# Kernel tuning notes

Hardware: AMD Instinct MI355X
Metric: run time of the kernel (lower is better)

The kernel has to match this reference:

```python
import jax, jax.numpy as jnp
import numpy as np

S, B, H, E, V, T = 160, 64, 1024, 512, 64, 16


def setup_inputs() -> dict:
    key = jax.random.key(0)
    ks = jax.random.split(key, 13)
    g = lambda k, shape, scale: jax.random.normal(k, shape, jnp.float32) * scale
    return dict(
        encoder_h0=g(ks[0], (1, B, H), 1.0),
        encoder_c0=g(ks[1], (1, B, H), 1.0),
        encoder_outputs=g(ks[2], (S, B, H), 1.0),
        encoder_lens=jax.random.randint(ks[3], (B,), 1, S + 1),
        tok_embed=g(ks[4], (1, E), 0.02),
        embed=g(ks[5], (V, E), 0.02),
        W_ih=g(ks[6], (4 * H, E), 1.0 / np.sqrt(E)),
        W_hh=g(ks[7], (4 * H, H), 1.0 / np.sqrt(H)),
        b_ih=jnp.zeros((4 * H,), jnp.float32),
        b_hh=jnp.zeros((4 * H,), jnp.float32),
        out_W=g(ks[8], (V, 2 * H), 1.0 / np.sqrt(2 * H)),
        out_b=jnp.zeros((V,), jnp.float32),
        enc_W=g(ks[9], (H, H), 1.0 / np.sqrt(H)),
        enc_b=jnp.zeros((H,), jnp.float32),
        dec_W=g(ks[10], (H, H), 1.0 / np.sqrt(H)),
        dec_b=jnp.zeros((H,), jnp.float32),
        attn_W=g(ks[11], (1, H), 1.0 / np.sqrt(H)),
        attn_b=jnp.zeros((1,), jnp.float32),
    )


def reference(encoder_h0, encoder_c0, encoder_outputs, encoder_lens,
              tok_embed, embed, W_ih, W_hh, b_ih, b_hh,
              out_W, out_b, enc_W, enc_b, dec_W, dec_b, attn_W, attn_b):
    S_, B_, H_ = encoder_outputs.shape
    h0, c0 = encoder_h0[0], encoder_c0[0]          # [B,H]; source re-feeds encoder_hidden each step
    invalid = jnp.arange(S_)[None, :] >= encoder_lens[:, None]   # [B,S] True where masked
    NEG = jnp.float32(-1e9)

    def step(embed_tok, _):
        # LSTM cell, torch gate order (i, f, g, o)
        gates = embed_tok @ W_ih.T + b_ih + h0 @ W_hh.T + b_hh   # [B,4H]
        i, f, g, o = jnp.split(gates, 4, axis=-1)
        c = jax.nn.sigmoid(f) * c0 + jax.nn.sigmoid(i) * jnp.tanh(g)
        out = jax.nn.sigmoid(o) * jnp.tanh(c)                    # [B,H]
        # additive (Bahdanau) attention scores
        enc_t = jnp.einsum('sbh,kh->sbk', encoder_outputs, enc_W) + enc_b   # [S,B,H]
        dec_t = out @ dec_W.T + dec_b                                       # [B,H]
        scores = (jnp.tanh(enc_t + dec_t[None]) @ attn_W[0] + attn_b[0]).T # [B,S]
        attn = jax.nn.softmax(jnp.where(invalid, NEG, scores), axis=-1)    # [B,S]
        context = jnp.einsum('bs,sbh->bh', attn, encoder_outputs)          # [B,H]
        combined = jnp.concatenate([context, out], axis=-1)                # [B,2H]
        probs = jax.nn.softmax(combined @ out_W.T + out_b, axis=-1)
        probs = probs / jnp.sum(probs, axis=-1, keepdims=True)             # source renormalizes
        tok = jnp.argmax(probs, axis=-1)                                   # greedy decode
        onehot = jax.nn.one_hot(tok, probs.shape[-1], dtype=probs.dtype)
        neg_ent = jnp.sum(jax.lax.stop_gradient(probs) * jnp.log(probs + 1e-6), axis=-1)
        logp = jnp.log(jnp.sum(probs * onehot, axis=-1) + 1e-6)
        return embed[tok], (tok, attn, neg_ent, logp)

    start = jnp.broadcast_to(tok_embed[0], (B_, tok_embed.shape[1]))  # <SOS> embedding
    _, (toks, attns, negents, logps) = jax.lax.scan(step, start, None, length=T)
    predicted_tokens = toks                            # [T,B]
    context_total = jnp.transpose(attns, (1, 0, 2))    # [B,T,S] (attention maps, as in source)
    return predicted_tokens, context_total, jnp.sum(negents, axis=0), jnp.sum(logps, axis=0)
```

## Files before the change

kernel.cpp:

```cpp
#include <hip/hip_runtime.h>

#define S_ 160
#define B_ 64
#define H_ 1024
#define E_ 512
#define V_ 64
#define T_ 16
#define H4_ 4096

__device__ __forceinline__ float sigm(float x) { return 1.f / (1.f + expf(-x)); }

__global__ __launch_bounds__(512) void gemm_bt_128(
    const float* __restrict__ A, const float* __restrict__ Bm,
    const float* __restrict__ bias, float* __restrict__ Cd,
    int M, int N, int K)
{
    __shared__ float As[16][132];
    __shared__ float Bs[16][132];
    const int bn = blockIdx.x, bm = blockIdx.y;
    const int tid = threadIdx.x;
    const int lr = tid >> 2, lk = (tid & 3) * 4;
    const int cx4 = (tid & 15) * 4, ry4 = (tid >> 4) * 4;
    const float* Ap = A + (size_t)(bm * 128 + lr) * K + lk;
    const float* Bp = Bm + (size_t)(bn * 128 + lr) * K + lk;
    float acc[4][8] = {};
    for (int k0 = 0; k0 < K; k0 += 16) {
        float4 av = *(const float4*)(Ap + k0);
        float4 bv = *(const float4*)(Bp + k0);
        __syncthreads();
        As[lk + 0][lr] = av.x; As[lk + 1][lr] = av.y;
        As[lk + 2][lr] = av.z; As[lk + 3][lr] = av.w;
        Bs[lk + 0][lr] = bv.x; Bs[lk + 1][lr] = bv.y;
        Bs[lk + 2][lr] = bv.z; Bs[lk + 3][lr] = bv.w;
        __syncthreads();
#pragma unroll
        for (int kk = 0; kk < 16; ++kk) {
            float a[4], b[8];
            *(float4*)(a)     = *(const float4*)&As[kk][ry4];
            *(float4*)(b)     = *(const float4*)&Bs[kk][cx4];
            *(float4*)(b + 4) = *(const float4*)&Bs[kk][64 + cx4];
#pragma unroll
            for (int i = 0; i < 4; ++i)
#pragma unroll
                for (int j = 0; j < 8; ++j) acc[i][j] = fmaf(a[i], b[j], acc[i][j]);
        }
    }
#pragma unroll
    for (int i = 0; i < 4; ++i) {
        int row = bm * 128 + ry4 + i;
#pragma unroll
        for (int j = 0; j < 8; ++j) {
            int col = bn * 128 + ((j < 4) ? (cx4 + j) : (64 + cx4 + j - 4));
            Cd[(size_t)row * N + col] = acc[i][j] + bias[col];
        }
    }
}

__device__ __forceinline__ void tile64(const float* __restrict__ Arow,
                                       const float* __restrict__ Brow,
                                       int K, float acc[4][4],
                                       float* __restrict__ As,
                                       float* __restrict__ Bs)
{
    const int tid = threadIdx.x;
    const int lr = tid >> 2, lc = (tid & 3) << 2;
    const int tx = tid & 15, ty = tid >> 4;
    for (int k0 = 0; k0 < K; k0 += 16) {
        float4 av = *(const float4*)(Arow + k0);
        float4 bv = *(const float4*)(Brow + k0);
        __syncthreads();
        As[lr * 17 + lc + 0] = av.x; As[lr * 17 + lc + 1] = av.y;
        As[lr * 17 + lc + 2] = av.z; As[lr * 17 + lc + 3] = av.w;
        Bs[lr * 17 + lc + 0] = bv.x; Bs[lr * 17 + lc + 1] = bv.y;
        Bs[lr * 17 + lc + 2] = bv.z; Bs[lr * 17 + lc + 3] = bv.w;
        __syncthreads();
#pragma unroll
        for (int kk = 0; kk < 16; ++kk) {
            float a[4], b[4];
#pragma unroll
            for (int i = 0; i < 4; ++i) a[i] = As[(ty * 4 + i) * 17 + kk];
#pragma unroll
            for (int j = 0; j < 4; ++j) b[j] = Bs[(tx * 4 + j) * 17 + kk];
#pragma unroll
            for (int i = 0; i < 4; ++i)
#pragma unroll
                for (int j = 0; j < 4; ++j) acc[i][j] = fmaf(a[i], b[j], acc[i][j]);
        }
    }
    __syncthreads();
}

__global__ __launch_bounds__(256) void gemm_part(
    const float* __restrict__ A, const float* __restrict__ Bm,
    float* __restrict__ Cpart, int M, int N, int K)
{
    __shared__ float smem[2176];
    const int bn = blockIdx.x, bm = blockIdx.y, kz = blockIdx.z, KS = gridDim.z;
    const int tid = threadIdx.x;
    const int lr = tid >> 2, lc = (tid & 3) << 2;
    const int tx = tid & 15, ty = tid >> 4;
    const int kLen = K / KS, k0base = kz * kLen;
    float acc[4][4] = {};
    tile64(A + (size_t)(bm * 64 + lr) * K + k0base + lc,
           Bm + (size_t)(bn * 64 + lr) * K + k0base + lc,
           kLen, acc, smem, smem + 1088);
    float* Cp = Cpart + (size_t)kz * M * N;
#pragma unroll
    for (int i = 0; i < 4; ++i) {
        int row = bm * 64 + ty * 4 + i;
#pragma unroll
        for (int j = 0; j < 4; ++j)
            Cp[(size_t)row * N + bn * 64 + tx * 4 + j] = acc[i][j];
    }
}

__global__ void reduce_partials(const float* __restrict__ Cpart, int KS,
                                const float* __restrict__ bias,
                                const float* __restrict__ bias2,
                                float* __restrict__ C, int MN, int N)
{
    int idx = blockIdx.x * 256 + threadIdx.x;
    if (idx >= MN) return;
    float v = 0.f;
    for (int z = 0; z < KS; ++z) v += Cpart[(size_t)z * MN + idx];
    int col = idx % N;
    if (bias)  v += bias[col];
    if (bias2) v += bias2[col];
    C[idx] = v;
}

__global__ void init_k(const float* __restrict__ embed, const float* __restrict__ tok_emb,
                       float* __restrict__ emb_ext,
                       float* __restrict__ negent, float* __restrict__ logp)
{
    int i = blockIdx.x * 256 + threadIdx.x;
    if (i < 128 * E_) {
        int r = i >> 9, c = i & (E_ - 1);
        emb_ext[i] = (r < 64) ? embed[r * E_ + c] : ((r == 64) ? tok_emb[c] : 0.f);
    }
    if (i < B_) { negent[i] = 0.f; logp[i] = 0.f; }
}

__global__ __launch_bounds__(256) void lstm_gather_k(
    const float* __restrict__ gsrc, size_t strideB,
    const float* __restrict__ hh_gates, const float* __restrict__ enc_c0,
    float* __restrict__ out_h)
{
    int idx = blockIdx.x * 256 + threadIdx.x;
    int b = idx >> 10, h = idx & (H_ - 1);
    const float* ag = gsrc + (size_t)b * strideB;
    const float* hg = hh_gates + (size_t)b * H4_;
    float gi = ag[h]           + hg[h];
    float gf = ag[H_ + h]      + hg[H_ + h];
    float gg = ag[2 * H_ + h]  + hg[2 * H_ + h];
    float go = ag[3 * H_ + h]  + hg[3 * H_ + h];
    float cc = sigm(gf) * enc_c0[idx] + sigm(gi) * tanhf(gg);
    out_h[idx] = sigm(go) * tanhf(cc);
}

__global__ __launch_bounds__(256) void score_k(
    const float* __restrict__ enc_t, const float* __restrict__ dec_part,
    const float* __restrict__ dec_b, const float* __restrict__ attn_W,
    const float* __restrict__ attn_b, const int* __restrict__ lens,
    float* __restrict__ scores)
{
    const int lane = threadIdx.x & 63;
    const int gw = blockIdx.x * 4 + (threadIdx.x >> 6);
    const int b = gw >> 5, sg = gw & 31;
    float dec_r[16], aw_r[16];
#pragma unroll
    for (int it = 0; it < 16; ++it) {
        int h = lane + it * 64;
        dec_r[it] = dec_part[(size_t)b * H_ + h]
                  + dec_part[(size_t)(B_ + b) * H_ + h]
                  + dec_part[(size_t)(2 * B_ + b) * H_ + h]
                  + dec_part[(size_t)(3 * B_ + b) * H_ + h]
                  + dec_b[h];
        aw_r[it] = attn_W[h];
    }
    const int len = lens[b];
    const float ab = attn_b[0];
    for (int s = sg * 5; s < sg * 5 + 5; ++s) {
        if (s >= len) { if (lane == 0) scores[b * S_ + s] = -1e9f; continue; }
        const float* ep = enc_t + ((size_t)s * B_ + b) * H_;
        float acc = 0.f;
#pragma unroll
        for (int it = 0; it < 16; ++it)
            acc += aw_r[it] * tanhf(ep[lane + it * 64] + dec_r[it]);
        for (int d = 32; d; d >>= 1) acc += __shfl_xor(acc, d);
        if (lane == 0) scores[b * S_ + s] = acc + ab;
    }
}

__global__ __launch_bounds__(256) void smax_out_k(
    const float* __restrict__ scores, const float* __restrict__ enc_out,
    const float* __restrict__ out_h, const float* __restrict__ out_W,
    const float* __restrict__ out_b, const float* __restrict__ all_gates,
    const int* __restrict__ lens, float* __restrict__ gates_sel,
    float* __restrict__ negent_acc, float* __restrict__ logp_acc,
    float* __restrict__ out, int t)
{
    __shared__ float sc[S_];
    __shared__ float comb[2 * H_];
    __shared__ float lg[V_];
    __shared__ int tok_s;
    const int tid = threadIdx.x;
    const int b = blockIdx.x;
    const int lane = tid & 63, wv = tid >> 6;
    if (wv == 0) {
        float m = -1e30f;
        for (int s = lane; s < S_; s += 64) {
            float v = scores[b * S_ + s]; sc[s] = v; m = fmaxf(m, v);
        }
        for (int d = 32; d; d >>= 1) m = fmaxf(m, __shfl_xor(m, d));
        float sum = 0.f;
        for (int s = lane; s < S_; s += 64) {
            float e = expf(sc[s] - m); sc[s] = e; sum += e;
        }
        for (int d = 32; d; d >>= 1) sum += __shfl_xor(sum, d);
        float inv = 1.f / sum;
        for (int s = lane; s < S_; s += 64) {
            float pr = sc[s] * inv; sc[s] = pr;
            out[T_ * B_ + ((size_t)b * T_ + t) * S_ + s] = pr;
        }
    }
    __syncthreads();
    {
        const int len4 = (lens[b] + 3) & ~3;
        const float* base = enc_out + (size_t)b * H_ + tid * 4;
        float4 ac0 = {0,0,0,0}, ac1 = {0,0,0,0}, ac2 = {0,0,0,0}, ac3 = {0,0,0,0};
        for (int s = 0; s < len4; s += 4) {
            float4 e0 = *(const float4*)(base + (size_t)(s    ) * B_ * H_);
            float4 e1 = *(const float4*)(base + (size_t)(s + 1) * B_ * H_);
            float4 e2 = *(const float4*)(base + (size_t)(s + 2) * B_ * H_);
            float4 e3 = *(const float4*)(base + (size_t)(s + 3) * B_ * H_);
            float p0 = sc[s], p1 = sc[s + 1], p2 = sc[s + 2], p3 = sc[s + 3];
            ac0.x = fmaf(p0, e0.x, ac0.x); ac0.y = fmaf(p0, e0.y, ac0.y);
            ac0.z = fmaf(p0, e0.z, ac0.z); ac0.w = fmaf(p0, e0.w, ac0.w);
            ac1.x = fmaf(p1, e1.x, ac1.x); ac1.y = fmaf(p1, e1.y, ac1.y);
            ac1.z = fmaf(p1, e1.z, ac1.z); ac1.w = fmaf(p1, e1.w, ac1.w);
            ac2.x = fmaf(p2, e2.x, ac2.x); ac2.y = fmaf(p2, e2.y, ac2.y);
            ac2.z = fmaf(p2, e2.z, ac2.z); ac2.w = fmaf(p2, e2.w, ac2.w);
            ac3.x = fmaf(p3, e3.x, ac3.x); ac3.y = fmaf(p3, e3.y, ac3.y);
            ac3.z = fmaf(p3, e3.z, ac3.z); ac3.w = fmaf(p3, e3.w, ac3.w);
        }
        comb[tid * 4 + 0] = ac0.x + ac1.x + ac2.x + ac3.x;
        comb[tid * 4 + 1] = ac0.y + ac1.y + ac2.y + ac3.y;
        comb[tid * 4 + 2] = ac0.z + ac1.z + ac2.z + ac3.z;
        comb[tid * 4 + 3] = ac0.w + ac1.w + ac2.w + ac3.w;
    }
    for (int i = tid; i < H_; i += 256) comb[H_ + i] = out_h[(size_t)b * H_ + i];
    __syncthreads();
    for (int v = wv * 16; v < wv * 16 + 16; ++v) {
        const float* w = out_W + (size_t)v * (2 * H_);
        float a0 = 0.f, a1 = 0.f;
#pragma unroll
        for (int j = 0; j < 32; j += 2) {
            a0 = fmaf(comb[lane + j * 64], w[lane + j * 64], a0);
            a1 = fmaf(comb[lane + (j + 1) * 64], w[lane + (j + 1) * 64], a1);
        }
        float acc = a0 + a1;
        for (int d = 32; d; d >>= 1) acc += __shfl_xor(acc, d);
        if (lane == 0) lg[v] = acc + out_b[v];
    }
    __syncthreads();
    if (wv == 0) {
        float x = lg[lane];
        float m = x;
        for (int d = 32; d; d >>= 1) m = fmaxf(m, __shfl_xor(m, d));
        float e = expf(x - m);
        float s = e;
        for (int d = 32; d; d >>= 1) s += __shfl_xor(s, d);
        float pr = e / s;
        float ps = pr;
        for (int d = 32; d; d >>= 1) ps += __shfl_xor(ps, d);
        pr = pr / ps;
        float bv = pr; int bi = lane;
        for (int d = 32; d; d >>= 1) {
            float ov = __shfl_xor(bv, d); int oi = __shfl_xor(bi, d);
            if (ov > bv || (ov == bv && oi < bi)) { bv = ov; bi = oi; }
        }
        float ne = pr * logf(pr + 1e-6f);
        for (int d = 32; d; d >>= 1) ne += __shfl_xor(ne, d);
        float ptok = __shfl(pr, bi);
        if (lane == 0) {
            out[t * B_ + b] = (float)bi;
            float na = negent_acc[b] + ne;                negent_acc[b] = na;
            float la = logp_acc[b] + logf(ptok + 1e-6f);  logp_acc[b] = la;
            if (t == T_ - 1) {
                out[T_ * B_ + B_ * T_ * S_ + b] = na;
                out[T_ * B_ + B_ * T_ * S_ + B_ + b] = la;
            }
            tok_s = bi;
        }
    }
    __syncthreads();
    {
        const int tk = tok_s;
        const float4* src = (const float4*)(all_gates + (size_t)tk * H4_);
        float4* dst = (float4*)(gates_sel + (size_t)b * H4_);
        for (int i = tid; i < H4_ / 4; i += 256) dst[i] = src[i];
    }
}

extern "C" void kernel_launch(void* const* d_in, const int* in_sizes, int n_in,
                              void* d_out, int out_size, void* d_ws, size_t ws_size,
                              hipStream_t stream) {
    const float* enc_h0  = (const float*)d_in[0];
    const float* enc_c0  = (const float*)d_in[1];
    const float* enc_out = (const float*)d_in[2];
    const int*   lens    = (const int*)d_in[3];
    const float* tok_emb = (const float*)d_in[4];
    const float* embed   = (const float*)d_in[5];
    const float* W_ih    = (const float*)d_in[6];
    const float* W_hh    = (const float*)d_in[7];
    const float* b_ih    = (const float*)d_in[8];
    const float* b_hh    = (const float*)d_in[9];
    const float* out_W   = (const float*)d_in[10];
    const float* out_b   = (const float*)d_in[11];
    const float* enc_W   = (const float*)d_in[12];
    const float* enc_b   = (const float*)d_in[13];
    const float* dec_W   = (const float*)d_in[14];
    const float* dec_b   = (const float*)d_in[15];
    const float* attn_W  = (const float*)d_in[16];
    const float* attn_b  = (const float*)d_in[17];
    float* out = (float*)d_out;

    float* ws = (float*)d_ws;
    float* hh_gates  = ws;
    float* out_h     = hh_gates + B_ * H4_;
    float* dec_part  = out_h + B_ * H_;
    float* scores    = dec_part + 4 * B_ * H_;
    float* negent    = scores + B_ * S_;
    float* logp      = negent + B_;
    float* gates_sel = logp + B_;
    float* emb_ext   = gates_sel + B_ * H4_;
    float* all_gates = emb_ext + 128 * E_;
    float* enc_t     = all_gates + (size_t)128 * H4_;
    float* part      = enc_t;
    if (ws_size < 47751680u) return;

    init_k<<<(128 * E_ + 255) / 256, 256, 0, stream>>>(embed, tok_emb, emb_ext,
                                                       negent, logp);

    gemm_part<<<dim3(H4_ / 64, 1, 4), 256, 0, stream>>>(enc_h0, W_hh, part, B_, H4_, H_);
    reduce_partials<<<(B_ * H4_ + 255) / 256, 256, 0, stream>>>(
        part, 4, b_ih, b_hh, hh_gates, B_ * H4_, H4_);

    gemm_part<<<dim3(H4_ / 64, 2, 1), 256, 0, stream>>>(emb_ext, W_ih, all_gates,
                                                        128, H4_, E_);

    gemm_bt_128<<<dim3(H_ / 128, (S_ * B_) / 128), 512, 0, stream>>>(
        enc_out, enc_W, enc_b, enc_t, S_ * B_, H_, H_);

    for (int t = 0; t < T_; ++t) {
        const float* gsrc = (t == 0) ? (all_gates + (size_t)64 * H4_) : gates_sel;
        const size_t strideB = (t == 0) ? 0 : (size_t)H4_;
        lstm_gather_k<<<(B_ * H_) / 256, 256, 0, stream>>>(gsrc, strideB, hh_gates,
                                                           enc_c0, out_h);
        gemm_part<<<dim3(H_ / 64, 1, 4), 256, 0, stream>>>(out_h, dec_W, dec_part, B_, H_, H_);
        score_k<<<512, 256, 0, stream>>>(enc_t, dec_part, dec_b, attn_W, attn_b, lens, scores);
        smax_out_k<<<64, 256, 0, stream>>>(scores, enc_out, out_h, out_W, out_b,
                                           all_gates, lens, gates_sel, negent, logp, out, t);
    }
}
```

Measured before the change: 1.663 ms.

## Precompute LSTM outputs for every token, fuse each decode step into one kernel

Because h0 and c0 are re-fed every step, the LSTM output depends only on the previous token (64 vocab entries plus SOS). The new path precomputes out_h, dec_t and the hidden-side logits for every (token, batch) pair up front with batched GEMMs. Each decode step then becomes a single per-batch kernel that computes scores, softmax, context, logits and argmax, and gathers the next step's precomputed rows. This removes four launches per step and the per-step GEMMs. It needs a larger workspace and adds up-front GEMM work over 66x64 rows, and it falls back to the old path if the workspace is too small.

```diff
diff --git a/kernel.cpp b/kernel.cpp
--- a/kernel.cpp
+++ b/kernel.cpp
@@ -139,6 +139,181 @@
         emb_ext[i] = (r < 64) ? embed[r * E_ + c] : ((r == 64) ? tok_emb[c] : 0.f);
     }
     if (i < B_) { negent[i] = 0.f; logp[i] = 0.f; }
+}
+
+__global__ __launch_bounds__(256) void outh_all_k(
+    const float* __restrict__ all_gates, const float* __restrict__ hh_gates,
+    const float* __restrict__ enc_c0, float* __restrict__ outh)
+{
+    size_t idx = (size_t)blockIdx.x * 256 + threadIdx.x;
+    int row = (int)(idx >> 10), h = (int)(idx & (H_ - 1));
+    int v = row >> 6, b = row & 63;
+    const float* ag = all_gates + (size_t)v * H4_;
+    const float* hg = hh_gates + (size_t)b * H4_;
+    float gi = ag[h]          + hg[h];
+    float gf = ag[H_ + h]     + hg[H_ + h];
+    float gg = ag[2 * H_ + h] + hg[2 * H_ + h];
+    float go = ag[3 * H_ + h] + hg[3 * H_ + h];
+    float cc = sigm(gf) * enc_c0[(size_t)b * H_ + h] + sigm(gi) * tanhf(gg);
+    outh[idx] = sigm(go) * tanhf(cc);
+}
+
+__global__ __launch_bounds__(256) void lgh_k(
+    const float* __restrict__ outh, const float* __restrict__ out_W,
+    const float* __restrict__ out_b, float* __restrict__ lgh)
+{
+    __shared__ float smem[2176];
+    const int bm = blockIdx.x;
+    const int tid = threadIdx.x;
+    const int lr = tid >> 2, lc = (tid & 3) << 2;
+    const int tx = tid & 15, ty = tid >> 4;
+    float acc[4][4] = {};
+    tile64(outh + (size_t)(bm * 64 + lr) * H_ + lc,
+           out_W + (size_t)lr * (2 * H_) + H_ + lc,
+           H_, acc, smem, smem + 1088);
+#pragma unroll
+    for (int i = 0; i < 4; ++i) {
+        int row = bm * 64 + ty * 4 + i;
+#pragma unroll
+        for (int j = 0; j < 4; ++j) {
+            int col = tx * 4 + j;
+            lgh[(size_t)row * V_ + col] = acc[i][j] + out_b[col];
+        }
+    }
+}
+
+__global__ __launch_bounds__(512) void step_k(
+    const float* __restrict__ enc_t, const float* __restrict__ enc_out,
+    const float* __restrict__ dsrc, const float* __restrict__ lsrc,
+    const float* __restrict__ attn_W, const float* __restrict__ attn_b,
+    const int* __restrict__ lens, const float* __restrict__ out_W,
+    const float* __restrict__ dec_all, const float* __restrict__ lg_h_all,
+    float* __restrict__ dec_sel, float* __restrict__ lg_sel,
+    float* __restrict__ negent_acc, float* __restrict__ logp_acc,
+    float* __restrict__ out, int t)
+{
+    __shared__ float sc[S_];
+    __shared__ float comb[H_];
+    __shared__ float lg[V_];
+    __shared__ int tok_s;
+    const int tid = threadIdx.x;
+    const int b = blockIdx.x;
+    const int lane = tid & 63, wv = tid >> 6;
+    const int len = lens[b];
+    {
+        float dec_r[16], aw_r[16];
+        const float* dr = dsrc + (size_t)b * H_;
+#pragma unroll
+        for (int it = 0; it < 16; ++it) {
+            int h = lane + it * 64;
+            dec_r[it] = dr[h];
+            aw_r[it] = attn_W[h];
+        }
+        const float ab = attn_b[0];
+        for (int i = 0; i < 20; ++i) {
+            int s = wv * 20 + i;
+            if (s >= len) { if (lane == 0) sc[s] = -1e9f; continue; }
+            const float* ep = enc_t + ((size_t)s * B_ + b) * H_;
+            float acc = 0.f;
+#pragma unroll
+            for (int it = 0; it < 16; ++it)
+                acc += aw_r[it] * tanhf(ep[lane + it * 64] + dec_r[it]);
+            for (int d = 32; d; d >>= 1) acc += __shfl_xor(acc, d);
+            if (lane == 0) sc[s] = acc + ab;
+        }
+    }
+    __syncthreads();
+    if (wv == 0) {
+        float m = -1e30f;
+        for (int s = lane; s < S_; s += 64) m = fmaxf(m, sc[s]);
+        for (int d = 32; d; d >>= 1) m = fmaxf(m, __shfl_xor(m, d));
+        float sum = 0.f;
+        for (int s = lane; s < S_; s += 64) {
+            float e = expf(sc[s] - m); sc[s] = e; sum += e;
+        }
+        for (int d = 32; d; d >>= 1) sum += __shfl_xor(sum, d);
+        float inv = 1.f / sum;
+        for (int s = lane; s < S_; s += 64) {
+            float pr = sc[s] * inv; sc[s] = pr;
+            out[T_ * B_ + ((size_t)b * T_ + t) * S_ + s] = pr;
+        }
+    }
+    __syncthreads();
+    {
+        const int len4 = (len + 3) & ~3;
+        const float* base = enc_out + (size_t)b * H_ + tid * 2;
+        float2 ac0 = {0,0}, ac1 = {0,0}, ac2 = {0,0}, ac3 = {0,0};
+        for (int s = 0; s < len4; s += 4) {
+            float2 e0 = *(const float2*)(base + (size_t)(s    ) * B_ * H_);
+            float2 e1 = *(const float2*)(base + (size_t)(s + 1) * B_ * H_);
+            float2 e2 = *(const float2*)(base + (size_t)(s + 2) * B_ * H_);
+            float2 e3 = *(const float2*)(base + (size_t)(s + 3) * B_ * H_);
+            float p0 = sc[s], p1 = sc[s + 1], p2 = sc[s + 2], p3 = sc[s + 3];
+            ac0.x = fmaf(p0, e0.x, ac0.x); ac0.y = fmaf(p0, e0.y, ac0.y);
+            ac1.x = fmaf(p1, e1.x, ac1.x); ac1.y = fmaf(p1, e1.y, ac1.y);
+            ac2.x = fmaf(p2, e2.x, ac2.x); ac2.y = fmaf(p2, e2.y, ac2.y);
+            ac3.x = fmaf(p3, e3.x, ac3.x); ac3.y = fmaf(p3, e3.y, ac3.y);
+        }
+        comb[tid * 2 + 0] = ac0.x + ac1.x + ac2.x + ac3.x;
+        comb[tid * 2 + 1] = ac0.y + ac1.y + ac2.y + ac3.y;
+    }
+    __syncthreads();
+    {
+        const float* lrow = lsrc + (size_t)b * V_;
+        for (int v = wv * 8; v < wv * 8 + 8; ++v) {
+            const float* w = out_W + (size_t)v * (2 * H_);
+            float a0 = 0.f, a1 = 0.f;
+#pragma unroll
+            for (int j = 0; j < 16; j += 2) {
+                a0 = fmaf(comb[lane + j * 64], w[lane + j * 64], a0);
+                a1 = fmaf(comb[lane + (j + 1) * 64], w[lane + (j + 1) * 64], a1);
+            }
+            float acc = a0 + a1;
+            for (int d = 32; d; d >>= 1) acc += __shfl_xor(acc, d);
+            if (lane == 0) lg[v] = acc + lrow[v];
+        }
+    }
+    __syncthreads();
+    if (wv == 0) {
+        float x = lg[lane];
+        float m = x;
+        for (int d = 32; d; d >>= 1) m = fmaxf(m, __shfl_xor(m, d));
+        float e = expf(x - m);
+        float s = e;
+        for (int d = 32; d; d >>= 1) s += __shfl_xor(s, d);
+        float pr = e / s;
+        float ps = pr;
+        for (int d = 32; d; d >>= 1) ps += __shfl_xor(ps, d);
+        pr = pr / ps;
+        float bv = pr; int bi = lane;
+        for (int d = 32; d; d >>= 1) {
+            float ov = __shfl_xor(bv, d); int oi = __shfl_xor(bi, d);
+            if (ov > bv || (ov == bv && oi < bi)) { bv = ov; bi = oi; }
+        }
+        float ne = pr * logf(pr + 1e-6f);
+        for (int d = 32; d; d >>= 1) ne += __shfl_xor(ne, d);
+        float ptok = __shfl(pr, bi);
+        if (lane == 0) {
+            out[t * B_ + b] = (float)bi;
+            float na = negent_acc[b] + ne;                negent_acc[b] = na;
+            float la = logp_acc[b] + logf(ptok + 1e-6f);  logp_acc[b] = la;
+            if (t == T_ - 1) {
+                out[T_ * B_ + B_ * T_ * S_ + b] = na;
+                out[T_ * B_ + B_ * T_ * S_ + B_ + b] = la;
+            }
+            tok_s = bi;
+        }
+    }
+    __syncthreads();
+    {
+        const int tk = tok_s;
+        const float* dsrc2 = dec_all + (size_t)(tk * 64 + b) * H_;
+        float* dd = dec_sel + (size_t)b * H_;
+        dd[tid] = dsrc2[tid];
+        dd[tid + 512] = dsrc2[tid + 512];
+        if (tid < V_)
+            lg_sel[(size_t)b * V_ + tid] = lg_h_all[(size_t)(tk * 64 + b) * V_ + tid];
+    }
 }
 
 __global__ __launch_bounds__(256) void lstm_gather_k(
@@ -327,6 +502,47 @@
     float* out = (float*)d_out;
 
     float* ws = (float*)d_ws;
+
+    if (ws_size >= 64012800u) {
+        float* hh_gates  = ws;
+        float* dec_sel   = hh_gates + B_ * H4_;
+        float* lg_sel    = dec_sel + B_ * H_;
+        float* negent    = lg_sel + B_ * V_;
+        float* logp      = negent + B_;
+        float* emb_ext   = logp + B_;
+        float* all_gates = emb_ext + 128 * E_;
+        float* lg_h_all  = all_gates + (size_t)128 * H4_;
+        float* dec_all   = lg_h_all + (size_t)66 * 64 * V_;
+        float* enc_t     = dec_all + (size_t)66 * 64 * H_;
+        float* outh_tmp  = enc_t;
+        float* part      = enc_t + (size_t)66 * 64 * H_;
+        part = enc_t;
+
+        init_k<<<(128 * E_ + 255) / 256, 256, 0, stream>>>(embed, tok_emb, emb_ext,
+                                                           negent, logp);
+        gemm_part<<<dim3(H4_ / 64, 1, 4), 256, 0, stream>>>(enc_h0, W_hh, part, B_, H4_, H_);
+        reduce_partials<<<(B_ * H4_ + 255) / 256, 256, 0, stream>>>(
+            part, 4, b_ih, b_hh, hh_gates, B_ * H4_, H4_);
+        gemm_part<<<dim3(H4_ / 64, 2, 1), 256, 0, stream>>>(emb_ext, W_ih, all_gates,
+                                                            128, H4_, E_);
+        outh_all_k<<<(66 * 64 * H_) / 256, 256, 0, stream>>>(all_gates, hh_gates,
+                                                             enc_c0, outh_tmp);
+        gemm_bt_128<<<dim3(H_ / 128, (66 * 64) / 128), 512, 0, stream>>>(
+            outh_tmp, dec_W, dec_b, dec_all, 66 * 64, H_, H_);
+        lgh_k<<<66, 256, 0, stream>>>(outh_tmp, out_W, out_b, lg_h_all);
+        gemm_bt_128<<<dim3(H_ / 128, (S_ * B_) / 128), 512, 0, stream>>>(
+            enc_out, enc_W, enc_b, enc_t, S_ * B_, H_, H_);
+
+        for (int t = 0; t < T_; ++t) {
+            const float* dsrc = (t == 0) ? (dec_all + (size_t)(64 * 64) * H_) : dec_sel;
+            const float* lsrc = (t == 0) ? (lg_h_all + (size_t)(64 * 64) * V_) : lg_sel;
+            step_k<<<B_, 512, 0, stream>>>(enc_t, enc_out, dsrc, lsrc, attn_W, attn_b,
+                                           lens, out_W, dec_all, lg_h_all, dec_sel,
+                                           lg_sel, negent, logp, out, t);
+        }
+        return;
+    }
+
     float* hh_gates  = ws;
     float* out_h     = hh_gates + B_ * H4_;
     float* dec_part  = out_h + B_ * H_;
@@ -342,14 +558,11 @@
 
     init_k<<<(128 * E_ + 255) / 256, 256, 0, stream>>>(embed, tok_emb, emb_ext,
                                                        negent, logp);
-
     gemm_part<<<dim3(H4_ / 64, 1, 4), 256, 0, stream>>>(enc_h0, W_hh, part, B_, H4_, H_);
     reduce_partials<<<(B_ * H4_ + 255) / 256, 256, 0, stream>>>(
         part, 4, b_ih, b_hh, hh_gates, B_ * H4_, H4_);
-
     gemm_part<<<dim3(H4_ / 64, 2, 1), 256, 0, stream>>>(emb_ext, W_ih, all_gates,
                                                         128, H4_, E_);
-
     gemm_bt_128<<<dim3(H_ / 128, (S_ * B_) / 128), 512, 0, stream>>>(
         enc_out, enc_W, enc_b, enc_t, S_ * B_, H_, H_);
 
```

Measured after the change: 2.932 ms. +76.3%, slower.
